# Performance work log

Hardware: AMD Instinct MI355X
Metric: run time of the kernel (lower is better)

Reference implementation:

```python
import jax, jax.numpy as jnp
import numpy as np

DIM = 1024
H = 16
HKV = 4
HD = DIM // H  # 64
GROUP = H // HKV
ROPE_BASE = 10000.0
B, T = 2, 2048


def rms_norm(x, eps):
    return x * jax.lax.rsqrt(jnp.mean(x * x, axis=-1, keepdims=True) + eps)


def apply_rotary(x, cos, sin):
    # x: [B, h, T, HD]; cos/sin: [1, 1, T, HD//2]
    half = x.shape[-1] // 2
    x1, x2 = x[..., :half], x[..., half:]
    return jnp.concatenate([x1 * cos + x2 * sin, -x1 * sin + x2 * cos], axis=-1)


def setup_inputs() -> dict:
    key = jax.random.key(0)
    ks = jax.random.split(key, 5)
    s = 0.02
    return {
        "x": jax.random.normal(ks[0], (B, T, DIM), dtype=jnp.float32),
        "Wq": jax.random.normal(ks[1], (DIM, DIM), dtype=jnp.float32) * s,
        "Wk": jax.random.normal(ks[2], (HKV * HD, DIM), dtype=jnp.float32) * s,
        "Wv": jax.random.normal(ks[3], (HKV * HD, DIM), dtype=jnp.float32) * s,
        "Wproj": jax.random.normal(ks[4], (DIM, DIM), dtype=jnp.float32) * s,
        "q_gain": jnp.full((H,), 12.0, dtype=jnp.float32),
    }


def reference(x, Wq, Wk, Wv, Wproj, q_gain):
    bsz, seqlen, dim = x.shape
    eps = jnp.asarray(jnp.finfo(x.dtype).eps, x.dtype)

    # double RMSNorm path: normalized input for q/k, raw input for v
    x_qk = rms_norm(x, eps)
    q = (x_qk @ Wq.T).reshape(bsz, seqlen, H, HD).transpose(0, 2, 1, 3)    # [B,H,T,D]
    k = (x_qk @ Wk.T).reshape(bsz, seqlen, HKV, HD).transpose(0, 2, 1, 3)  # [B,Hkv,T,D]
    v = (x @ Wv.T).reshape(bsz, seqlen, HKV, HD).transpose(0, 2, 1, 3)     # [B,Hkv,T,D]

    q = rms_norm(q, eps)
    k = rms_norm(k, eps)

    # rotary embeddings
    t = jnp.arange(seqlen, dtype=jnp.float32)
    inv_freq = 1.0 / (ROPE_BASE ** (jnp.arange(0, HD, 2, dtype=jnp.float32) / HD))
    freqs = jnp.outer(t, inv_freq)                       # [T, HD//2]
    cos = jnp.cos(freqs)[None, None].astype(x.dtype)
    sin = jnp.sin(freqs)[None, None].astype(x.dtype)
    q = apply_rotary(q, cos, sin)
    k = apply_rotary(k, cos, sin)

    # per-head gain on q
    q = q * q_gain.astype(q.dtype)[None, :, None, None]

    # GQA: expand kv heads to query heads
    k_r = jnp.repeat(k, GROUP, axis=1)  # [B,H,T,D]
    v_r = jnp.repeat(v, GROUP, axis=1)

    scale = 1.0 / np.sqrt(HD)
    scores = jnp.einsum("bhqd,bhkd->bhqk", q, k_r) * scale
    causal = jnp.tril(jnp.ones((seqlen, seqlen), dtype=bool))
    scores = jnp.where(causal[None, None], scores, jnp.asarray(-jnp.inf, scores.dtype))
    attn = jax.nn.softmax(scores, axis=-1)
    y = jnp.einsum("bhqk,bhkd->bhqd", attn, v_r)          # [B,H,T,D]

    # XSA: remove value-direction component from output
    y_bt = y.transpose(0, 2, 1, 3)                        # [B,T,H,D]
    v_bt = v.transpose(0, 2, 1, 3)                        # [B,T,Hkv,D]
    y_g = y_bt.reshape(bsz, seqlen, HKV, GROUP, HD)
    vnorm = jnp.sqrt(jnp.sum(v_bt * v_bt, axis=-1, keepdims=True))
    vn = (v_bt / jnp.maximum(vnorm, 1e-12))[..., None, :]  # [B,T,Hkv,1,D]
    proj = jnp.sum(y_g * vn, axis=-1, keepdims=True) * vn
    y_bt = (y_g - proj).reshape(bsz, seqlen, H, HD)

    return y_bt.reshape(bsz, seqlen, dim) @ Wproj.T
```

## Files before the change

### kernel.cpp

```cpp
#include <hip/hip_runtime.h>
#include <hip/hip_bf16.h>

typedef __attribute__((ext_vector_type(8))) short bf8v;
typedef __attribute__((ext_vector_type(4))) float f4v;

#define MFMA16(a,b,c) __builtin_amdgcn_mfma_f32_16x16x32_bf16((a),(b),(c),0,0,0)

#define GLD16(gp, lp) __builtin_amdgcn_global_load_lds( \
    (const __attribute__((address_space(1))) void*)(gp), \
    (__attribute__((address_space(3))) void*)(lp), 16, 0, 0)

#define DIMC   1024
#define TSEQ   2048
#define NH     16
#define NKV    4
#define HDIM   64
#define RMS_EPS 1.1920929e-07f
#define QSCALE 0.1803368801111601f

__device__ __forceinline__ ushort f2bf(float f) {
  unsigned u = __builtin_bit_cast(unsigned, f);
  u = (u + 0x7FFFu + ((u >> 16) & 1u)) >> 16;
  return (ushort)u;
}
__device__ __forceinline__ float bf2f(ushort u) {
  return __builtin_bit_cast(float, (unsigned)u << 16);
}
__device__ __forceinline__ unsigned cvtpk(float lo, float hi) {
  unsigned r;
  asm("v_cvt_pk_bf16_f32 %0, %1, %2" : "=v"(r) : "v"(lo), "v"(hi));
  return r;
}

__global__ __launch_bounds__(256) void prep_all(
    const float* __restrict__ x,
    const float* __restrict__ Wq, const float* __restrict__ Wk,
    const float* __restrict__ Wv, const float* __restrict__ Wp,
    ushort* __restrict__ xhi, ushort* __restrict__ xlo,
    ushort* __restrict__ xb,
    ushort* __restrict__ wqkh, ushort* __restrict__ wqkl,
    ushort* __restrict__ wvb, ushort* __restrict__ wpb,
    float* __restrict__ cosT, float* __restrict__ sinT) {
  __shared__ float red[4];
  int bid = blockIdx.x, tid = threadIdx.x;
  if (bid < 4096) {
    int row = bid;
    int lane = tid & 63, w = tid >> 6;
    float4 v = ((const float4*)(x + (size_t)row * DIMC))[tid];
    float ss = v.x * v.x + v.y * v.y + v.z * v.z + v.w * v.w;
    for (int off = 32; off; off >>= 1) ss += __shfl_xor(ss, off);
    if (lane == 0) red[w] = ss;
    __syncthreads();
    float tot = red[0] + red[1] + red[2] + red[3];
    float rs = rsqrtf(tot * (1.0f / DIMC) + RMS_EPS);
    float n0 = v.x * rs, n1 = v.y * rs, n2 = v.z * rs, n3 = v.w * rs;
    ushort4 h, l, ob;
    h.x = f2bf(n0); l.x = f2bf(n0 - bf2f(h.x));
    h.y = f2bf(n1); l.y = f2bf(n1 - bf2f(h.y));
    h.z = f2bf(n2); l.z = f2bf(n2 - bf2f(h.z));
    h.w = f2bf(n3); l.w = f2bf(n3 - bf2f(h.w));
    ob.x = f2bf(v.x); ob.y = f2bf(v.y); ob.z = f2bf(v.z); ob.w = f2bf(v.w);
    ((ushort4*)(xhi + (size_t)row * DIMC))[tid] = h;
    ((ushort4*)(xlo + (size_t)row * DIMC))[tid] = l;
    ((ushort4*)(xb  + (size_t)row * DIMC))[tid] = ob;
    return;
  }
  int wb = bid - 4096;
  if (wb < 1280) {
    const float* src;
    size_t si, di;
    if (wb < 1024) { src = Wq; si = (size_t)wb * 256 + tid; di = si; }
    else { src = Wk; si = (size_t)(wb - 1024) * 256 + tid; di = 262144 + si; }
    float4 v = ((const float4*)src)[si];
    ushort4 h, l;
    h.x = f2bf(v.x); l.x = f2bf(v.x - bf2f(h.x));
    h.y = f2bf(v.y); l.y = f2bf(v.y - bf2f(h.y));
    h.z = f2bf(v.z); l.z = f2bf(v.z - bf2f(h.z));
    h.w = f2bf(v.w); l.w = f2bf(v.w - bf2f(h.w));
    ((ushort4*)wqkh)[di] = h;
    ((ushort4*)wqkl)[di] = l;
  } else if (wb < 2560) {
    const float* src;
    ushort* dst;
    int i;
    if (wb < 1536) { src = Wv; dst = wvb; i = (wb - 1280) * 256 + tid; }
    else           { src = Wp; dst = wpb; i = (wb - 1536) * 256 + tid; }
    float4 v = ((const float4*)src)[i];
    ushort4 o;
    o.x = f2bf(v.x); o.y = f2bf(v.y); o.z = f2bf(v.z); o.w = f2bf(v.w);
    ((ushort4*)dst)[i] = o;
  } else {
    int i = (wb - 2560) * 256 + tid;
    int t = i >> 5, j = i & 31;
    float inv = 1.0f / powf(10000.0f, (float)j * (1.0f / 32.0f));
    float f = (float)t * inv;
    cosT[i] = cosf(f);
    sinT[i] = sinf(f);
  }
}

__global__ __launch_bounds__(256, 3)
void gemm_qkv(const ushort* __restrict__ xhi, const ushort* __restrict__ xlo,
              const ushort* __restrict__ wqkh, const ushort* __restrict__ wqkl,
              float* __restrict__ QKf, ushort* __restrict__ QKc,
              const ushort* __restrict__ xb, const ushort* __restrict__ wvb,
              float* __restrict__ Vf) {
  __shared__ __align__(16) ushort lA[128 * 64];
  __shared__ __align__(16) ushort lB[128 * 64];
  const int bid = blockIdx.x;
  int u;
  bool big;
  if (bid < 256)      { big = true;  u = bid; }
  else if (bid < 448) { big = false; u = bid - 256; }
  else if (bid < 512) { big = true;  u = 256 + (bid - 448); }
  else                { big = false; u = 192 + (bid - 512); }

  const ushort *Ap0, *Bp0, *Ap1, *Bp1;
  float* Cf = QKf;
  int N = 1280, nsteps, mt, n0;
  if (big) {
    mt = u / 10; n0 = (u % 10) * 128;
    Ap0 = xlo; Bp0 = wqkh; Ap1 = xhi; Bp1 = wqkl; nsteps = 32;
  } else if (u < 320) {
    mt = u / 10; n0 = (u % 10) * 128;
    Ap0 = xhi; Bp0 = wqkh; Ap1 = Ap0; Bp1 = Bp0; nsteps = 16;
  } else {
    int v = u - 320; mt = v >> 1; n0 = (v & 1) * 128;
    Ap0 = xb; Bp0 = wvb; Ap1 = Ap0; Bp1 = Bp0; nsteps = 16;
    Cf = Vf; N = 256;
  }
  const int m0 = mt * 128;

  const int t = threadIdx.x;
  const int lane = t & 63, w = t >> 6;
  const int wr = w >> 1, wc = w & 1;
  const int l15 = lane & 15, lg = lane >> 4;
  const int srow = t >> 3, scp = t & 7;

  f4v acc[4][4] = {};

  for (int s = 0; s < nsteps; ++s) {
    const ushort* Ab = (s < 16) ? Ap0 : Ap1;
    const ushort* Bb = (s < 16) ? Bp0 : Bp1;
    const int kk = (s & 15) * 64;
    for (int i = 0; i < 4; ++i) {
      int row = srow + i * 32;
      int sc = scp ^ (row & 7);
      const ushort* ga = Ab + (size_t)(m0 + row) * DIMC + kk + sc * 8;
      const ushort* gb = Bb + (size_t)(n0 + row) * DIMC + kk + sc * 8;
      GLD16(ga, &lA[w * 512 + i * 2048]);
      GLD16(gb, &lB[w * 512 + i * 2048]);
    }
    __syncthreads();
    for (int kx = 0; kx < 2; ++kx) {
      bf8v af[4], bfr[4];
      for (int m = 0; m < 4; ++m) {
        int row = wr * 64 + m * 16 + l15;
        int ch = (kx * 4 + lg) ^ (row & 7);
        af[m] = *(const bf8v*)&lA[row * 64 + ch * 8];
      }
      for (int n = 0; n < 4; ++n) {
        int row = wc * 64 + n * 16 + l15;
        int ch = (kx * 4 + lg) ^ (row & 7);
        bfr[n] = *(const bf8v*)&lB[row * 64 + ch * 8];
      }
      for (int m = 0; m < 4; ++m)
        for (int n = 0; n < 4; ++n)
          acc[m][n] = MFMA16(af[m], bfr[n], acc[m][n]);
    }
    __syncthreads();
  }

  if (big) {
    for (int m = 0; m < 4; ++m)
      for (int n = 0; n < 4; ++n)
        for (int j = 0; j < 4; ++j) {
          int r = m0 + wr * 64 + m * 16 + lg * 4 + j;
          int c = n0 + wc * 64 + n * 16 + l15;
          QKc[(size_t)r * 1280 + c] = f2bf(acc[m][n][j]);
        }
  } else {
    for (int m = 0; m < 4; ++m)
      for (int n = 0; n < 4; ++n)
        for (int j = 0; j < 4; ++j) {
          int r = m0 + wr * 64 + m * 16 + lg * 4 + j;
          int c = n0 + wc * 64 + n * 16 + l15;
          Cf[(size_t)r * N + c] = acc[m][n][j];
        }
  }
}

__global__ __launch_bounds__(256, 2)
void gemm_bt(const ushort* __restrict__ A0, const ushort* __restrict__ B0,
             float* __restrict__ C, int N) {
  __shared__ __align__(16) ushort lA[128 * 64];
  __shared__ __align__(16) ushort lB[128 * 64];
  const int t = threadIdx.x;
  const int lane = t & 63, w = t >> 6;
  const int wr = w >> 1, wc = w & 1;
  const int l15 = lane & 15, lg = lane >> 4;
  const int m0 = blockIdx.y * 128, n0 = blockIdx.x * 128;
  const int srow = t >> 3, scp = t & 7;

  f4v acc[4][4] = {};

  for (int k0 = 0; k0 < 1024; k0 += 64) {
    for (int i = 0; i < 4; ++i) {
      int row = srow + i * 32;
      int sc = scp ^ (row & 7);
      const ushort* ga = A0 + (size_t)(m0 + row) * DIMC + k0 + sc * 8;
      const ushort* gb = B0 + (size_t)(n0 + row) * DIMC + k0 + sc * 8;
      GLD16(ga, &lA[w * 512 + i * 2048]);
      GLD16(gb, &lB[w * 512 + i * 2048]);
    }
    __syncthreads();
    for (int kx = 0; kx < 2; ++kx) {
      bf8v af[4], bfr[4];
      for (int m = 0; m < 4; ++m) {
        int row = wr * 64 + m * 16 + l15;
        int ch = (kx * 4 + lg) ^ (row & 7);
        af[m] = *(const bf8v*)&lA[row * 64 + ch * 8];
      }
      for (int n = 0; n < 4; ++n) {
        int row = wc * 64 + n * 16 + l15;
        int ch = (kx * 4 + lg) ^ (row & 7);
        bfr[n] = *(const bf8v*)&lB[row * 64 + ch * 8];
      }
      for (int m = 0; m < 4; ++m)
        for (int n = 0; n < 4; ++n)
          acc[m][n] = MFMA16(af[m], bfr[n], acc[m][n]);
    }
    __syncthreads();
  }

  for (int m = 0; m < 4; ++m)
    for (int n = 0; n < 4; ++n)
      for (int j = 0; j < 4; ++j) {
        int r = m0 + wr * 64 + m * 16 + lg * 4 + j;
        int c = n0 + wc * 64 + n * 16 + l15;
        C[(size_t)r * N + c] = acc[m][n][j];
      }
}

__global__ __launch_bounds__(256) void post_all(
    const float* __restrict__ QKf, const ushort* __restrict__ QKc,
    const float* __restrict__ cosT,
    const float* __restrict__ sinT, const float* __restrict__ qgain,
    ushort* __restrict__ qhi, ushort* __restrict__ qlo,
    ushort* __restrict__ kb16,
    const float* __restrict__ Vf, ushort* __restrict__ vt2,
    ushort* __restrict__ vhat_q) {
  __shared__ float lds[64][69];
  __shared__ float rnv[64];
  int bid = blockIdx.x;
  if (bid < 4096) {
    int m = bid;
    int b = m >> 11, tpos = m & 2047;
    int lane = threadIdx.x & 63, w = threadIdx.x >> 6;
    int d = lane, j = d & 31;
    float sgn = (d < 32) ? 1.0f : -1.0f;
    float c = cosT[tpos * 32 + j], s = sinT[tpos * 32 + j];

    for (int i = 0; i < 4; ++i) {
      int h = w * 4 + i;
      size_t base = (size_t)m * 1280 + h * HDIM + d;
      float q = QKf[base] + bf2f(QKc[base]);
      float ss = q * q;
      for (int off = 32; off; off >>= 1) ss += __shfl_xor(ss, off);
      float rs = rsqrtf(ss * (1.0f / HDIM) + RMS_EPS);
      float qn = q * rs;
      float partner = __shfl_xor(qn, 32);
      float ro = (qn * c + sgn * partner * s) * (qgain[h] * QSCALE);
      ushort hi = f2bf(ro);
      ushort lo = f2bf(ro - bf2f(hi));
      size_t idx = (((size_t)b * NH + h) * TSEQ + tpos) * HDIM + d;
      qhi[idx] = hi;
      qlo[idx] = lo;
    }
    {
      int kv = w;
      size_t base = (size_t)m * 1280 + 1024 + kv * HDIM + d;
      float k = QKf[base] + bf2f(QKc[base]);
      float ss = k * k;
      for (int off = 32; off; off >>= 1) ss += __shfl_xor(ss, off);
      float rs = rsqrtf(ss * (1.0f / HDIM) + RMS_EPS);
      float kn = k * rs;
      float partner = __shfl_xor(kn, 32);
      float ro = kn * c + sgn * partner * s;
      kb16[((size_t)(b * NKV + kv) * TSEQ + tpos) * HDIM + d] = f2bf(ro);
    }
    return;
  }
  {
    int vb = bid - 4096;
    int bkv = vb >> 5, tt = vb & 31;
    int b = bkv >> 2, kv = bkv & 3;
    int tid = threadIdx.x;
    for (int i = 0; i < 16; ++i) {
      int idx = i * 256 + tid;
      int tloc = idx >> 6, d = idx & 63;
      lds[d][tloc] = Vf[((size_t)(b * TSEQ + tt * 64 + tloc)) * 256 + kv * 64 + d];
    }
    __syncthreads();
    {
      int t = tid >> 2, prt = tid & 3;
      float ssum = 0.f;
      for (int dd = 0; dd < 16; ++dd) {
        float v = lds[prt * 16 + dd][t];
        ssum += v * v;
      }
      ssum += __shfl_xor(ssum, 1);
      ssum += __shfl_xor(ssum, 2);
      if (prt == 0) rnv[t] = 1.0f / fmaxf(sqrtf(ssum), 1e-12f);
    }
    __syncthreads();
    for (int i = 0; i < 16; ++i) {
      int idx = i * 256 + tid;
      int d = idx >> 6, tloc = idx & 63;
      vt2[(size_t)bkv * (TSEQ * 64) + tt * 4096 + d * 64 + tloc] = f2bf(lds[d][tloc]);
    }
    for (int i = 0; i < 16; ++i) {
      int idx = i * 256 + tid;
      int tloc = idx >> 6, d = idx & 63;
      vhat_q[((size_t)bkv * TSEQ + tt * 64 + tloc) * 64 + d] =
          f2bf(lds[d][tloc] * rnv[tloc]);
    }
  }
}

#define E(s,t,k,l) ((unsigned)(s) | ((unsigned)(t) << 8) | \
                    ((unsigned)(k) << 16) | ((unsigned)(l) << 24))
__global__ __launch_bounds__(256, 5) void attn_chunk(
    const ushort* __restrict__ qhi, const ushort* __restrict__ qlo,
    const ushort* __restrict__ kb16, const ushort* __restrict__ vt2,
    ushort* __restrict__ pyb, float* __restrict__ pml) {
  static const unsigned LUT[80] = {
    E(76,31,0,8), E(77,31,8,8), E(78,31,16,8), E(79,31,24,8),
    E(72,30,0,8), E(73,30,8,8), E(74,30,16,8),
    E(68,29,0,8), E(69,29,8,8), E(64,28,0,8),
    E(45,23,0,8), E(46,23,8,8), E(47,23,16,8),
    E(42,22,0,8), E(43,22,8,8), E(39,21,0,8),
    E(22,15,0,8), E(23,15,8,8), E(20,14,0,8), E(7,7,0,8),
    E(75,30,24,7), E(70,29,16,7), E(71,29,23,7),
    E(65,28,8,7), E(66,28,15,7), E(67,28,22,7),
    E(60,27,0,7), E(61,27,7,7), E(62,27,14,7), E(63,27,21,7),
    E(56,26,0,7), E(57,26,7,7), E(58,26,14,7),
    E(52,25,0,7), E(53,25,7,7), E(48,24,0,7),
    E(44,22,16,7), E(40,21,8,7), E(41,21,15,7),
    E(36,20,0,7), E(37,20,7,7), E(38,20,14,7),
    E(33,19,0,7), E(34,19,7,7), E(30,18,0,7),
    E(21,14,8,7), E(18,13,0,7), E(19,13,7,7), E(16,12,0,7), E(6,6,0,7),
    E(59,26,21,6), E(54,25,14,6), E(55,25,20,6),
    E(49,24,7,6), E(50,24,13,6), E(51,24,19,6),
    E(35,19,14,6), E(31,18,7,6), E(32,18,13,6),
    E(27,17,0,6), E(28,17,6,6), E(29,17,12,6),
    E(24,16,0,6), E(25,16,6,6),
    E(17,12,7,6), E(14,11,0,6), E(15,11,6,6), E(12,10,0,6), E(5,5,0,6),
    E(26,16,12,5), E(13,10,6,5), E(10,9,0,5), E(11,9,5,5),
    E(8,8,0,5), E(4,4,0,5),
    E(9,8,5,4), E(3,3,0,4),
    E(2,2,0,3), E(1,1,0,2), E(0,0,0,1)
  };
  __shared__ __align__(16) ushort lk[2][64 * 64];
  __shared__ __align__(16) ushort lv[2][64 * 64];
  const int t = threadIdx.x;
  const int lane = t & 63, w = t >> 6;
  const int bid = blockIdx.x;
  const int combo = bid & 31;
  const unsigned e = LUT[bid >> 5];
  const int slot = e & 255;
  const int tile = (e >> 8) & 31;
  const int kb0 = (e >> 16) & 31;
  const int len = (int)(e >> 24);

  const int xcd = combo & 7, g = (combo >> 3) & 3;
  const int b = xcd >> 2, kv = xcd & 3, h = kv * 4 + g;
  const int l15 = lane & 15, lg = lane >> 4;
  const int q0 = tile * 64 + w * 16;
  const int t3 = t >> 3, tc8 = t & 7;
  const int rx = l15 & 7;
  const int pswz = rx << 2;

  const size_t qoff = (((size_t)(b * NH + h)) * TSEQ + q0 + l15) * HDIM;
  bf8v bq0h = *(const bf8v*)(qhi + qoff + lg * 8);
  bf8v bq1h = *(const bf8v*)(qhi + qoff + 32 + lg * 8);
  bf8v bq0l = *(const bf8v*)(qlo + qoff + lg * 8);
  bf8v bq1l = *(const bf8v*)(qlo + qoff + 32 + lg * 8);

  const ushort* kb = kb16 + (size_t)(b * NKV + kv) * TSEQ * 64;
  const ushort* vb = vt2 + (size_t)(b * NKV + kv) * TSEQ * 64;

#define STAGE(BUF, KT) do { \
    _Pragma("unroll") \
    for (int i = 0; i < 2; ++i) { \
      int row = i * 32 + t3; \
      int sc = tc8 ^ (row & 7); \
      GLD16(kb + (size_t)((KT) * 64 + row) * 64 + sc * 8, \
            &lk[BUF][(i * 32 + (w << 3)) * 64]); \
      GLD16(vb + (size_t)(KT) * 4096 + row * 64 + sc * 8, \
            &lv[BUF][(i * 32 + (w << 3)) * 64]); \
    } } while (0)

  STAGE(0, kb0);

  f4v y[4] = {};
  float mrow = -1e30f, lrow = 0.f;

#pragma unroll 1
  for (int itc = 0; itc < len; ++itc) {
    const int cur = itc & 1;
    const int kt = kb0 + itc;
    __syncthreads();
    if (itc + 1 < len) STAGE(cur ^ 1, kt + 1);

    const ushort* lkc = &lk[cur][0];
    const ushort* lvc = &lv[cur][0];
    unsigned* pw = (unsigned*)&lk[cur][w << 10];
    const int kv0 = kt * 64;

    f4v s4[4];
    __builtin_amdgcn_s_setprio(1);
#pragma unroll
    for (int n = 0; n < 4; ++n) {
      const ushort* krow = lkc + (n * 16 + l15) * 64;
      bf8v kh0 = *(const bf8v*)&krow[((0 + lg) ^ rx) * 8];
      bf8v kh1 = *(const bf8v*)&krow[((4 + lg) ^ rx) * 8];
      f4v z = {};
      f4v acc = MFMA16(kh0, bq0h, z);
      acc = MFMA16(kh1, bq1h, acc);
      acc = MFMA16(kh0, bq0l, acc);
      acc = MFMA16(kh1, bq1l, acc);
      s4[n] = acc;
    }
    __builtin_amdgcn_s_setprio(0);

    const bool need_mask = (kt == tile);
    float mloc = -1e30f;
#pragma unroll
    for (int n = 0; n < 4; ++n)
#pragma unroll
      for (int j = 0; j < 4; ++j) {
        float v = s4[n][j];
        if (need_mask && (kv0 + n * 16 + lg * 4 + j > q0 + l15)) v = -1e30f;
        s4[n][j] = v;
        mloc = fmaxf(mloc, v);
      }
    if (__any(mloc > mrow + 11.5f)) {
      float mf = fmaxf(mloc, __shfl_xor(mloc, 16));
      mf = fmaxf(mf, __shfl_xor(mf, 32));
      float mnew = fmaxf(mrow, mf);
      float scf = exp2f(mrow - mnew);
      lrow *= scf;
#pragma unroll
      for (int n = 0; n < 4; ++n) y[n] *= scf;
      mrow = mnew;
    }
#pragma unroll
    for (int n = 0; n < 4; ++n)
#pragma unroll
      for (int j = 0; j < 4; ++j) {
        float e2 = exp2f(s4[n][j] - mrow);
        s4[n][j] = e2;
        lrow += e2;
      }

    asm volatile("s_waitcnt lgkmcnt(0)" ::: "memory");
    __builtin_amdgcn_s_barrier();

#pragma unroll
    for (int n = 0; n < 4; ++n) {
      uint2 pk;
      pk.x = cvtpk(s4[n][0], s4[n][1]);
      pk.y = cvtpk(s4[n][2], s4[n][3]);
      *(uint2*)&pw[l15 * 32 + ((8 * n + 2 * lg) ^ pswz)] = pk;
    }
    asm volatile("s_waitcnt lgkmcnt(0)" ::: "memory");
    bf8v pb0 = *(const bf8v*)&pw[l15 * 32 + ((lg * 4) ^ pswz)];
    bf8v pb1 = *(const bf8v*)&pw[l15 * 32 + ((16 + lg * 4) ^ pswz)];
    __builtin_amdgcn_s_setprio(1);
#pragma unroll
    for (int n = 0; n < 4; ++n) {
      const ushort* vrow = lvc + (n * 16 + l15) * 64;
      bf8v va0 = *(const bf8v*)&vrow[((0 + lg) ^ rx) * 8];
      bf8v va1 = *(const bf8v*)&vrow[((4 + lg) ^ rx) * 8];
      y[n] = MFMA16(va0, pb0, y[n]);
      y[n] = MFMA16(va1, pb1, y[n]);
    }
    __builtin_amdgcn_s_setprio(0);
  }
#undef STAGE

  {
    lrow += __shfl_xor(lrow, 16);
    lrow += __shfl_xor(lrow, 32);
    const int pslot = combo * 80 + slot;
    ushort* pb = pyb + (size_t)pslot * 4096;
    const int q = w * 16 + l15;
#pragma unroll
    for (int n = 0; n < 4; ++n) {
      uint2 pk;
      pk.x = cvtpk(y[n][0], y[n][1]);
      pk.y = cvtpk(y[n][2], y[n][3]);
      *(uint2*)&pb[q * 64 + n * 16 + lg * 4] = pk;
    }
    if (lane < 16) {
      float* mlp = pml + (size_t)pslot * 128;
      mlp[q] = mrow;
      mlp[64 + q] = lrow;
    }
  }
}
#undef E

__global__ __launch_bounds__(256) void combine_kern(
    const ushort* __restrict__ pyb, const float* __restrict__ pml,
    const ushort* __restrict__ vhat_q, ushort* __restrict__ ytil) {
  const int bid = blockIdx.x;
  const int combo = bid & 31, tile = bid >> 5;
  const int xcd = combo & 7, g = (combo >> 3) & 3;
  const int b = xcd >> 2, kv = xcd & 3, h = kv * 4 + g;
  const int nch = (tile + 8) >> 3;
  const int sb = (tile < 8) ? tile
               : (tile < 16) ? 8 + ((tile - 8) << 1)
               : (tile < 24) ? 24 + 3 * (tile - 16)
                             : 48 + ((tile - 24) << 2);
  const int tid = threadIdx.x;
  const int q = tid >> 2, ds = (tid & 3) * 16;
  const int q0 = tile * 64;

  float m[4], l[4];
#pragma unroll
  for (int ci = 0; ci < 4; ++ci) {
    if (ci < nch) {
      const float* mlp = pml + (size_t)(combo * 80 + sb + ci) * 128;
      m[ci] = mlp[q];
      l[ci] = mlp[64 + q];
    } else { m[ci] = -1e30f; l[ci] = 0.f; }
  }
  float M = fmaxf(fmaxf(m[0], m[1]), fmaxf(m[2], m[3]));
  float y[16] = {};
  float ltot = 0.f;
#pragma unroll
  for (int ci = 0; ci < 4; ++ci) {
    if (ci < nch) {
      float sc = exp2f(m[ci] - M);
      ltot += l[ci] * sc;
      const ushort* pb = pyb + (size_t)(combo * 80 + sb + ci) * 4096 + q * 64 + ds;
      bf8v p0 = *(const bf8v*)pb;
      bf8v p1 = *(const bf8v*)(pb + 8);
#pragma unroll
      for (int dd = 0; dd < 8; ++dd) {
        y[dd] += sc * bf2f((ushort)p0[dd]);
        y[8 + dd] += sc * bf2f((ushort)p1[dd]);
      }
    }
  }
  float inv = 1.0f / ltot;
  const ushort* vh = vhat_q + ((size_t)(b * NKV + kv) * TSEQ + q0 + q) * 64 + ds;
  bf8v v0 = *(const bf8v*)vh;
  bf8v v1 = *(const bf8v*)(vh + 8);
  float vv[16];
  float dp = 0.f;
#pragma unroll
  for (int dd = 0; dd < 8; ++dd) {
    vv[dd] = bf2f((ushort)v0[dd]);
    vv[8 + dd] = bf2f((ushort)v1[dd]);
  }
#pragma unroll
  for (int dd = 0; dd < 16; ++dd) {
    y[dd] *= inv;
    dp += y[dd] * vv[dd];
  }
  dp += __shfl_xor(dp, 1);
  dp += __shfl_xor(dp, 2);
  bf8v o0, o1;
#pragma unroll
  for (int dd = 0; dd < 8; ++dd) {
    o0[dd] = (short)f2bf(y[dd] - dp * vv[dd]);
    o1[dd] = (short)f2bf(y[8 + dd] - dp * vv[8 + dd]);
  }
  ushort* yo = ytil + ((size_t)(b * TSEQ + q0 + q)) * DIMC + h * HDIM + ds;
  *(bf8v*)yo = o0;
  *(bf8v*)(yo + 8) = o1;
}

extern "C" void kernel_launch(void* const* d_in, const int* in_sizes, int n_in,
                              void* d_out, int out_size, void* d_ws, size_t ws_size,
                              hipStream_t stream) {
  (void)in_sizes; (void)n_in; (void)out_size; (void)ws_size;
  const float* x  = (const float*)d_in[0];
  const float* Wq = (const float*)d_in[1];
  const float* Wk = (const float*)d_in[2];
  const float* Wv = (const float*)d_in[3];
  const float* Wp = (const float*)d_in[4];
  const float* qg = (const float*)d_in[5];
  float* out = (float*)d_out;
  char* ws = (char*)d_ws;
  const size_t KB = 1024, MB = 1ull << 20;

  ushort* xhi = (ushort*)(ws);
  ushort* xlo = (ushort*)(ws + 8 * MB);
  ushort* xb  = (ushort*)(ws + 16 * MB);
  ushort* wqkh = (ushort*)(ws + 24 * MB);
  ushort* wqkl = (ushort*)(ws + 26 * MB + 512 * KB);
  ushort* wvb = (ushort*)(ws + 29 * MB);
  ushort* wpb = (ushort*)(ws + 29 * MB + 512 * KB);
  float*  cosT = (float*)(ws + 31 * MB + 512 * KB);
  float*  sinT = (float*)(ws + 31 * MB + 768 * KB);
  float*  QKf  = (float*)(ws + 32 * MB);
  ushort* kb16 = (ushort*)(ws + 52 * MB);
  ushort* vt2  = (ushort*)(ws + 54 * MB);

  float*  Vf   = out;
  ushort* QKc  = (ushort*)((char*)out + 4 * MB);
  ushort* vhat_q = (ushort*)((char*)out + 14 * MB);
  ushort* qhb  = xhi;
  ushort* qlb  = xlo;
  ushort* ytil = xb;
  ushort* pyb = (ushort*)(ws + 32 * MB);
  float*  pml = (float*)(ws + 56 * MB);

  prep_all<<<6912, 256, 0, stream>>>(x, Wq, Wk, Wv, Wp, xhi, xlo, xb,
                                     wqkh, wqkl, wvb, wpb, cosT, sinT);

  gemm_qkv<<<704, 256, 0, stream>>>(xhi, xlo, wqkh, wqkl, QKf, QKc,
                                    xb, wvb, Vf);

  post_all<<<4352, 256, 0, stream>>>(QKf, QKc, cosT, sinT, qg, qhb, qlb, kb16,
                                     Vf, vt2, vhat_q);
  attn_chunk<<<2560, 256, 0, stream>>>(qhb, qlb, kb16, vt2, pyb, pml);
  combine_kern<<<1024, 256, 0, stream>>>(pyb, pml, vhat_q, ytil);
  gemm_bt<<<dim3(8, 32), 256, 0, stream>>>(ytil, wpb, out, 1024);
}
```

Measured before the change: 144.7 us.

## Shrink output GEMM tile and replace LDS P transpose with lane permutes

The output projection GEMM moves from 128x128 to 128x64 tiles, doubling the grid to 512 blocks so more of the machine is busy on this small GEMM. In the attention kernel, the softmax probabilities are now rearranged into MFMA B-operand layout with v_permlane32_swap and shfl_xor lane exchanges instead of a round trip through LDS. That also drops an s_barrier and the lgkmcnt waits per KV tile. The trade-off is more cross-lane instructions, and the smaller GEMM tile gives less operand reuse per block.

```diff
diff --git a/kernel.cpp b/kernel.cpp
--- a/kernel.cpp
+++ b/kernel.cpp
@@ -3,6 +3,7 @@
 
 typedef __attribute__((ext_vector_type(8))) short bf8v;
 typedef __attribute__((ext_vector_type(4))) float f4v;
+typedef __attribute__((ext_vector_type(4))) unsigned u4v;
 
 #define MFMA16(a,b,c) __builtin_amdgcn_mfma_f32_16x16x32_bf16((a),(b),(c),0,0,0)
 
@@ -194,50 +195,53 @@
 void gemm_bt(const ushort* __restrict__ A0, const ushort* __restrict__ B0,
              float* __restrict__ C, int N) {
   __shared__ __align__(16) ushort lA[128 * 64];
-  __shared__ __align__(16) ushort lB[128 * 64];
+  __shared__ __align__(16) ushort lB[64 * 64];
   const int t = threadIdx.x;
   const int lane = t & 63, w = t >> 6;
-  const int wr = w >> 1, wc = w & 1;
   const int l15 = lane & 15, lg = lane >> 4;
-  const int m0 = blockIdx.y * 128, n0 = blockIdx.x * 128;
+  const int m0 = blockIdx.y * 128, n0 = blockIdx.x * 64;
   const int srow = t >> 3, scp = t & 7;
 
-  f4v acc[4][4] = {};
+  f4v acc[2][4] = {};
 
   for (int k0 = 0; k0 < 1024; k0 += 64) {
     for (int i = 0; i < 4; ++i) {
       int row = srow + i * 32;
       int sc = scp ^ (row & 7);
       const ushort* ga = A0 + (size_t)(m0 + row) * DIMC + k0 + sc * 8;
+      GLD16(ga, &lA[w * 512 + i * 2048]);
+    }
+    for (int i = 0; i < 2; ++i) {
+      int row = srow + i * 32;
+      int sc = scp ^ (row & 7);
       const ushort* gb = B0 + (size_t)(n0 + row) * DIMC + k0 + sc * 8;
-      GLD16(ga, &lA[w * 512 + i * 2048]);
       GLD16(gb, &lB[w * 512 + i * 2048]);
     }
     __syncthreads();
     for (int kx = 0; kx < 2; ++kx) {
-      bf8v af[4], bfr[4];
-      for (int m = 0; m < 4; ++m) {
-        int row = wr * 64 + m * 16 + l15;
+      bf8v af[2], bfr[4];
+      for (int m = 0; m < 2; ++m) {
+        int row = w * 32 + m * 16 + l15;
         int ch = (kx * 4 + lg) ^ (row & 7);
         af[m] = *(const bf8v*)&lA[row * 64 + ch * 8];
       }
       for (int n = 0; n < 4; ++n) {
-        int row = wc * 64 + n * 16 + l15;
+        int row = n * 16 + l15;
         int ch = (kx * 4 + lg) ^ (row & 7);
         bfr[n] = *(const bf8v*)&lB[row * 64 + ch * 8];
       }
-      for (int m = 0; m < 4; ++m)
+      for (int m = 0; m < 2; ++m)
         for (int n = 0; n < 4; ++n)
           acc[m][n] = MFMA16(af[m], bfr[n], acc[m][n]);
     }
     __syncthreads();
   }
 
-  for (int m = 0; m < 4; ++m)
+  for (int m = 0; m < 2; ++m)
     for (int n = 0; n < 4; ++n)
       for (int j = 0; j < 4; ++j) {
-        int r = m0 + wr * 64 + m * 16 + lg * 4 + j;
-        int c = n0 + wc * 64 + n * 16 + l15;
+        int r = m0 + w * 32 + m * 16 + lg * 4 + j;
+        int c = n0 + n * 16 + l15;
         C[(size_t)r * N + c] = acc[m][n][j];
       }
 }
@@ -379,7 +383,7 @@
   const int q0 = tile * 64 + w * 16;
   const int t3 = t >> 3, tc8 = t & 7;
   const int rx = l15 & 7;
-  const int pswz = rx << 2;
+  const bool odd = (lg & 1);
 
   const size_t qoff = (((size_t)(b * NH + h)) * TSEQ + q0 + l15) * HDIM;
   bf8v bq0h = *(const bf8v*)(qhi + qoff + lg * 8);
@@ -415,7 +419,6 @@
 
     const ushort* lkc = &lk[cur][0];
     const ushort* lvc = &lv[cur][0];
-    unsigned* pw = (unsigned*)&lk[cur][w << 10];
     const int kv0 = kt * 64;
 
     f4v s4[4];
@@ -464,19 +467,29 @@
         lrow += e2;
       }
 
-    asm volatile("s_waitcnt lgkmcnt(0)" ::: "memory");
-    __builtin_amdgcn_s_barrier();
-
-#pragma unroll
-    for (int n = 0; n < 4; ++n) {
-      uint2 pk;
-      pk.x = cvtpk(s4[n][0], s4[n][1]);
-      pk.y = cvtpk(s4[n][2], s4[n][3]);
-      *(uint2*)&pw[l15 * 32 + ((8 * n + 2 * lg) ^ pswz)] = pk;
-    }
-    asm volatile("s_waitcnt lgkmcnt(0)" ::: "memory");
-    bf8v pb0 = *(const bf8v*)&pw[l15 * 32 + ((lg * 4) ^ pswz)];
-    bf8v pb1 = *(const bf8v*)&pw[l15 * 32 + ((16 + lg * 4) ^ pswz)];
+    unsigned d0a = cvtpk(s4[0][0], s4[0][1]), d0b = cvtpk(s4[0][2], s4[0][3]);
+    unsigned d1a = cvtpk(s4[1][0], s4[1][1]), d1b = cvtpk(s4[1][2], s4[1][3]);
+    unsigned d2a = cvtpk(s4[2][0], s4[2][1]), d2b = cvtpk(s4[2][2], s4[2][3]);
+    unsigned d3a = cvtpk(s4[3][0], s4[3][1]), d3b = cvtpk(s4[3][2], s4[3][3]);
+    asm("v_permlane32_swap_b32 %0, %1" : "+v"(d0a), "+v"(d1a));
+    asm("v_permlane32_swap_b32 %0, %1" : "+v"(d0b), "+v"(d1b));
+    asm("v_permlane32_swap_b32 %0, %1" : "+v"(d2a), "+v"(d3a));
+    asm("v_permlane32_swap_b32 %0, %1" : "+v"(d2b), "+v"(d3b));
+    unsigned sa0 = (unsigned)__shfl_xor((int)d0a, 16);
+    unsigned sb0 = (unsigned)__shfl_xor((int)d1a, 16);
+    unsigned sa1 = (unsigned)__shfl_xor((int)d0b, 16);
+    unsigned sb1 = (unsigned)__shfl_xor((int)d1b, 16);
+    unsigned sa2 = (unsigned)__shfl_xor((int)d2a, 16);
+    unsigned sb2 = (unsigned)__shfl_xor((int)d3a, 16);
+    unsigned sa3 = (unsigned)__shfl_xor((int)d2b, 16);
+    unsigned sb3 = (unsigned)__shfl_xor((int)d3b, 16);
+    u4v u0 = { odd ? sb0 : d0a, odd ? sb1 : d0b,
+               odd ? d1a : sa0, odd ? d1b : sa1 };
+    u4v u1 = { odd ? sb2 : d2a, odd ? sb3 : d2b,
+               odd ? d3a : sa2, odd ? d3b : sa3 };
+    bf8v pb0 = __builtin_bit_cast(bf8v, u0);
+    bf8v pb1 = __builtin_bit_cast(bf8v, u1);
+
     __builtin_amdgcn_s_setprio(1);
 #pragma unroll
     for (int n = 0; n < 4; ++n) {
@@ -630,5 +643,5 @@
                                      Vf, vt2, vhat_q);
   attn_chunk<<<2560, 256, 0, stream>>>(qhb, qlb, kb16, vt2, pyb, pml);
   combine_kern<<<1024, 256, 0, stream>>>(pyb, pml, vhat_q, ytil);
-  gemm_bt<<<dim3(8, 32), 256, 0, stream>>>(ytil, wpb, out, 1024);
-}
+  gemm_bt<<<dim3(16, 32), 256, 0, stream>>>(ytil, wpb, out, 1024);
+}
```

After: 141.9 us. Within noise of the previous version (-1.9%).
